# Performance work log

Hardware: AMD Instinct MI355X
Metric: run time of the kernel (lower is better)

The kernel has to match this reference:

```python
import jax, jax.numpy as jnp
import numpy as np

B, T, D = 1, 1024, 1024
H = 16; HKV = 16; HD = D // H; R = 2; K = 3; LOWR = 32
HR = HKV * R                      # heads after harmonic expansion
OUTW = HKV * HD * 2 * R           # w_proj output width
SCALE = HD ** -0.5


def setup_inputs() -> dict:
    key = jax.random.key(0)
    ks = jax.random.split(key, 10)
    def rn(k, shape, sc=1.0):
        return jax.random.normal(k, shape, dtype=jnp.float32) * sc
    return {
        'hidden_states': rn(ks[0], (B, T, D)),
        'q_w': rn(ks[1], (D, D), D ** -0.5),
        'k_w': rn(ks[2], (D, D), D ** -0.5),
        'v_w': rn(ks[3], (D, D), D ** -0.5),
        'w1': rn(ks[4], (LOWR, D), D ** -0.5),
        'w2': rn(ks[5], (OUTW, LOWR), LOWR ** -0.5),
        'conv_w': rn(ks[6], (OUTW, K), K ** -0.5),
        'bt_w': rn(ks[7], (HKV * R, D), D ** -0.5),
        'bt_b': jnp.zeros((HKV * R,), jnp.float32),
        'o_w': rn(ks[8], (D, D * R), (D * R) ** -0.5),
        'omega': 0.01 * jnp.ones((1, 1, 1, R), jnp.float32),
        'phi': jnp.zeros((1, 1, 1, R), jnp.float32),
    }


def path_attention_forward(hidden_states, q_w, k_w, v_w, w1, w2, conv_w,
                           bt_w, bt_b, o_w, omega, phi):
    b, t, _ = hidden_states.shape
    q = hidden_states @ q_w.T
    k = hidden_states @ k_w.T
    v = hidden_states @ v_w.T
    # low-rank w projection, causal depthwise short conv (kernel K), SiLU
    w_raw = (hidden_states @ w1.T) @ w2.T                    # [b,t,OUTW]
    xp = jnp.pad(w_raw, ((0, 0), (K - 1, 0), (0, 0)))
    w_raw = sum(xp[:, i:i + t, :] * conv_w[:, i] for i in range(K))
    w_raw = jax.nn.silu(w_raw)
    # rotary-like harmonic mixing of Householder directions
    w5 = w_raw.reshape(b, t, HKV, 2 * R, HD)
    Ah = w5[:, :, :, 0::2, :]                                # [b,t,HKV,R,HD]
    Bh = w5[:, :, :, 1::2, :]
    pos = jnp.arange(t, dtype=jnp.float32)[None, :, None, None]
    theta = omega * pos + phi                                # [1,t,1,R]
    c = jnp.cos(theta)[..., None]
    s = jnp.sin(theta)[..., None]
    Wdir = Ah * c + Bh * s
    Wdir = Wdir * jax.lax.rsqrt(jnp.sum(Wdir * Wdir, -1, keepdims=True) + 1e-6)
    beta = jax.nn.sigmoid(hidden_states @ bt_w.T + bt_b) * 2.0   # [b,t,HR]
    # repeat-interleave q/k/v heads across harmonics -> [b,HR,t,HD]
    to_h = lambda x: jnp.swapaxes(jnp.repeat(x.reshape(b, t, H, HD), R, axis=2), 1, 2)
    qh, kh, vh = to_h(q), to_h(k), to_h(v)
    wh = jnp.swapaxes(Wdir.reshape(b, t, HR, HD), 1, 2)      # [b,HR,t,HD]
    bh = jnp.swapaxes(beta, 1, 2)                            # [b,HR,t]
    # PaTH logits: A_ij = q_i^T (H_i ... H_{j+1}) k_j, H_t = I - beta_t w_t w_t^T.
    # WY/UT transform: with M_ts = beta_t (w_t.w_s) for s<t, the coefficients
    # B_tj (t>j) of the accumulated rank-1 corrections solve the unit-lower
    # triangular system (I + M) B = strilow(Db W K^T), and
    # A = tril(Q K^T - tril(Q W^T) B).
    idx = jnp.arange(t)
    strict = idx[:, None] > idx[None, :]
    incl = idx[:, None] >= idx[None, :]
    Mw = jnp.where(strict, jnp.einsum('bhtd,bhsd->bhts', wh, wh) * bh[..., None], 0.0)
    rhs = jnp.where(strict, jnp.einsum('bhtd,bhjd->bhtj', wh, kh) * bh[..., None], 0.0)
    Bmat = jax.scipy.linalg.solve_triangular(Mw + jnp.eye(t, dtype=Mw.dtype), rhs, lower=True)
    qk = jnp.einsum('bhid,bhjd->bhij', qh, kh)
    qw = jnp.where(incl, jnp.einsum('bhid,bhtd->bhit', qh, wh), 0.0)
    logits = (qk - jnp.einsum('bhit,bhtj->bhij', qw, Bmat)) * SCALE
    logits = jnp.where(incl, logits, -1e30)
    p = jax.nn.softmax(logits, axis=-1)
    o = jnp.einsum('bhij,bhjd->bhid', p, vh)                 # [b,HR,t,HD]
    o = jnp.swapaxes(o, 1, 2).reshape(b, t, HR * HD)         # [b,t,D*R]
    return o @ o_w.T


def reference(hidden_states, q_w, k_w, v_w, w1, w2, conv_w, bt_w, bt_b, o_w, omega, phi):
    return path_attention_forward(hidden_states, q_w, k_w, v_w, w1, w2, conv_w,
                                  bt_w, bt_b, o_w, omega, phi)
```

## Files before the change

kernel.cpp:

```cpp
#include <hip/hip_runtime.h>
#include <math.h>

#define TTD 1024
#define DDM 1024
#define HDIM 64
#define NOUTW 4096
#define PSCALE 0.125f
#define LS 72

typedef __attribute__((ext_vector_type(8))) __bf16 bf16x8;
typedef __attribute__((ext_vector_type(4))) float f32x4;
#define MFMA16(a,b,c) __builtin_amdgcn_mfma_f32_16x16x32_bf16(a,b,c,0,0,0)

__device__ __forceinline__ ushort f2b(float f) {
  unsigned u = __builtin_bit_cast(unsigned, f);
  return (ushort)((u + 0x7fffu + ((u >> 16) & 1u)) >> 16);
}
__device__ __forceinline__ float b2f(ushort u) {
  unsigned v = (unsigned)u << 16;
  return __builtin_bit_cast(float, v);
}

__device__ __forceinline__ void gload_lds16(const ushort* g, ushort* l) {
  __builtin_amdgcn_global_load_lds(
      (const __attribute__((address_space(1))) unsigned*)g,
      (__attribute__((address_space(3))) unsigned*)l, 16, 0, 0);
}

#define SWZ(row, cc) (((row) * 8 + ((cc) ^ ((row) & 7))) * 8)
#define SWZE(row, col) (SWZ(row, (col) >> 3) + ((col) & 7))

__device__ __forceinline__ void stage_tile(const ushort* gb, long gs, ushort* tile,
                                           int w, int l) {
  int sub = l >> 3, cc = (l & 7) ^ sub;
  #pragma unroll
  for (int it = 0; it < 2; ++it) {
    int q = w * 2 + it;
    gload_lds16(gb + (long)(q * 8 + sub) * gs + cc * 8, &tile[(q * 64 + l) * 8]);
  }
}

__device__ __forceinline__ bf16x8 frag(const ushort* tile, int row, int cc) {
  return *(const bf16x8*)&tile[SWZ(row, cc)];
}

#define OFF_X     0L
#define OFF_PZ    67108864L
#define OFF_HSB   67108864L
#define OFF_QWW   69206016L
#define OFF_KWW   71303168L
#define OFF_VWW   73400320L
#define OFF_W2B   75497472L
#define OFF_WLOWB 75759616L
#define OFF_TB    130023424L
#define OFF_OALL  130023424L
#define OFF_YB    134217728L
#define OFF_OWB   134217728L
#define OFF_WHB   138412032L
#define OFF_QB    142606336L
#define OFF_KB    144703488L
#define OFF_VTB   146800640L
#define OFF_BETA  148897792L
#define OFF_BW64  149159936L

__global__ __launch_bounds__(256) void cvt_kernel(const float* __restrict__ x,
                                                  ushort* __restrict__ y, long n) {
  long i = ((long)blockIdx.x * 256 + threadIdx.x) * 4;
  if (i >= n) return;
  float4 f = *(const float4*)(x + i);
  ushort4 o;
  o.x = f2b(f.x); o.y = f2b(f.y); o.z = f2b(f.z); o.w = f2b(f.w);
  *(ushort4*)(y + i) = o;
}

#define CVT_TOTAL 4358144L
struct CvtSegs {
  const float* src[6];
  ushort* dst[6];
  long cnt[6];
};
__global__ __launch_bounds__(256) void cvt_all_kernel(CvtSegs sg) {
  long e = ((long)blockIdx.x * 256 + threadIdx.x) * 4;
  #pragma unroll
  for (int s = 0; s < 6; ++s) {
    if (e < sg.cnt[s]) {
      float4 f = *(const float4*)(sg.src[s] + e);
      ushort4 o;
      o.x = f2b(f.x); o.y = f2b(f.y); o.z = f2b(f.z); o.w = f2b(f.w);
      *(ushort4*)(sg.dst[s] + e) = o;
      return;
    }
    e -= sg.cnt[s];
  }
}

__global__ __launch_bounds__(256) void qkv_sp_kernel(
    const ushort* __restrict__ hsb,
    const ushort* __restrict__ wq, const ushort* __restrict__ wk, const ushort* __restrict__ wv,
    const ushort* __restrict__ bw, const float* __restrict__ bt_b,
    ushort* __restrict__ cq, ushort* __restrict__ ck, ushort* __restrict__ cv,
    float* __restrict__ beta, ushort* __restrict__ wlowb)
{
  int z = blockIdx.z;
  if (z == 3 && blockIdx.x != 0) return;
  const ushort* B = (z == 0) ? wq : (z == 1) ? wk : (z == 2) ? wv : bw;

  __shared__ ushort Ab[2][8192];
  __shared__ ushort Bb[2][4096];

  int tid = threadIdx.x, w = tid >> 6, l = tid & 63;
  int quad = l >> 4, lane15 = l & 15;
  int rm = blockIdx.y * 128, cn = (z == 3) ? 0 : blockIdx.x * 64;
  const ushort* Ag = hsb + (long)rm * DDM;
  const ushort* Bg = B + (long)cn * DDM;

  stage_tile(Ag, DDM, &Ab[0][0], w, l);
  stage_tile(Ag + 64 * DDM, DDM, &Ab[0][4096], w, l);
  stage_tile(Bg, DDM, &Bb[0][0], w, l);
  __syncthreads();

  f32x4 acc[2][4] = {};
  int cur = 0;
  int arow0 = (w & 1) * 32 + lane15;
  int asel = (w >> 1) * 4096;
  for (int kt = 0; kt < 16; ++kt) {
    if (kt < 15) {
      stage_tile(Ag + (kt + 1) * 64, DDM, &Ab[cur ^ 1][0], w, l);
      stage_tile(Ag + 64 * DDM + (kt + 1) * 64, DDM, &Ab[cur ^ 1][4096], w, l);
      stage_tile(Bg + (kt + 1) * 64, DDM, &Bb[cur ^ 1][0], w, l);
    }
    const ushort* Atile = &Ab[cur][asel];
    #pragma unroll
    for (int s = 0; s < 2; ++s) {
      bf16x8 a0 = frag(Atile, arow0, s * 4 + quad);
      bf16x8 a1 = frag(Atile, arow0 + 16, s * 4 + quad);
      #pragma unroll
      for (int f = 0; f < 4; ++f) {
        bf16x8 bf = frag(&Bb[cur][0], f * 16 + lane15, s * 4 + quad);
        acc[0][f] = MFMA16(a0, bf, acc[0][f]);
        acc[1][f] = MFMA16(a1, bf, acc[1][f]);
      }
    }
    __syncthreads();
    cur ^= 1;
  }

  if (z < 2) {
    ushort* Cb = (z == 0) ? cq : ck;
    #pragma unroll
    for (int rr = 0; rr < 2; ++rr) {
      int orow = rm + w * 32 + rr * 16 + quad * 4;
      #pragma unroll
      for (int f = 0; f < 4; ++f)
        #pragma unroll
        for (int r = 0; r < 4; ++r)
          Cb[(long)(orow + r) * DDM + cn + f * 16 + lane15] = f2b(acc[rr][f][r]);
    }
  } else if (z == 2) {
    #pragma unroll
    for (int rr = 0; rr < 2; ++rr) {
      int orow = rm + w * 32 + rr * 16 + quad * 4;
      #pragma unroll
      for (int f = 0; f < 4; ++f) {
        ushort4 o;
        o.x = f2b(acc[rr][f][0]); o.y = f2b(acc[rr][f][1]);
        o.z = f2b(acc[rr][f][2]); o.w = f2b(acc[rr][f][3]);
        *(ushort4*)&cv[(long)(cn + f * 16 + lane15) * TTD + orow] = o;
      }
    }
  } else {
    #pragma unroll
    for (int rr = 0; rr < 2; ++rr) {
      int orow = rm + w * 32 + rr * 16 + quad * 4;
      #pragma unroll
      for (int f = 0; f < 2; ++f) {
        int hr = f * 16 + lane15;
        float bb = bt_b[hr];
        #pragma unroll
        for (int r = 0; r < 4; ++r)
          beta[(long)hr * TTD + orow + r] = 2.f / (1.f + expf(-(acc[rr][f][r] + bb)));
      }
      #pragma unroll
      for (int f = 2; f < 4; ++f)
        #pragma unroll
        for (int r = 0; r < 4; ++r)
          wlowb[(long)(orow + r) * 32 + (f - 2) * 16 + lane15] = f2b(acc[rr][f][r]);
    }
  }
}

__global__ __launch_bounds__(256) void wrawconv_kernel(
    const ushort* __restrict__ wlowb, const ushort* __restrict__ w2b,
    const float* __restrict__ conv_w, const float* __restrict__ omega,
    const float* __restrict__ phi, ushort* __restrict__ whb)
{
  int rm = blockIdx.x * 64;
  int p = blockIdx.y;
  int hkv = p >> 1, r = p & 1;
  int c0 = hkv * 256 + r * 128;

  __shared__ ushort As[64 * 32];
  __shared__ ushort Bs[128 * 32];
  __shared__ float WR[66][132];

  int tid = threadIdx.x, w = tid >> 6, l = tid & 63;
  int quad = l >> 4, lane15 = l & 15;

  {
    int row = tid >> 2, ch = (tid & 3) * 8;
    gload_lds16(wlowb + (long)(rm + row) * 32 + ch, &As[row * 32 + ch]);
    gload_lds16(w2b + (long)(c0 + row) * 32 + ch, &Bs[row * 32 + ch]);
    gload_lds16(w2b + (long)(c0 + 64 + row) * 32 + ch, &Bs[(64 + row) * 32 + ch]);
  }
  {
    int hr2 = tid >> 7, col = tid & 127;
    float acc = 0.f;
    if (rm > 0) {
      long t = rm - 2 + hr2;
      for (int k = 0; k < 32; ++k)
        acc += b2f(wlowb[t * 32 + k]) * b2f(w2b[(long)(c0 + col) * 32 + k]);
    }
    WR[hr2][col] = acc;
  }
  __syncthreads();

  #pragma unroll
  for (int g = 0; g < 2; ++g) {
    f32x4 acc[4] = {};
    bf16x8 af = *(const bf16x8*)&As[(w * 16 + lane15) * 32 + quad * 8];
    #pragma unroll
    for (int f = 0; f < 4; ++f) {
      bf16x8 bf = *(const bf16x8*)&Bs[(g * 64 + f * 16 + lane15) * 32 + quad * 8];
      acc[f] = MFMA16(af, bf, acc[f]);
    }
    #pragma unroll
    for (int f = 0; f < 4; ++f)
      #pragma unroll
      for (int rr = 0; rr < 4; ++rr)
        WR[2 + w * 16 + quad * 4 + rr][g * 64 + f * 16 + lane15] = acc[f][rr];
  }
  __syncthreads();

  float cwa[3], cwb[3];
  #pragma unroll
  for (int i = 0; i < 3; ++i) {
    cwa[i] = conv_w[(long)(c0 + l) * 3 + i];
    cwb[i] = conv_w[(long)(c0 + 64 + l) * 3 + i];
  }
  float om = omega[r], ph = phi[r];
  for (int it = 0; it < 16; ++it) {
    int tl = it * 4 + w;
    int t = rm + tl;
    float a = cwa[0] * WR[tl][l] + cwa[1] * WR[tl + 1][l] + cwa[2] * WR[tl + 2][l];
    float b = cwb[0] * WR[tl][64 + l] + cwb[1] * WR[tl + 1][64 + l] + cwb[2] * WR[tl + 2][64 + l];
    a = a / (1.f + expf(-a));
    b = b / (1.f + expf(-b));
    float th = om * (float)t + ph;
    float wd = a * cosf(th) + b * sinf(th);
    float ss = wd * wd;
    #pragma unroll
    for (int o = 32; o > 0; o >>= 1) ss += __shfl_xor(ss, o, 64);
    whb[((long)p * TTD + t) * HDIM + l] = f2b(wd * (1.f / sqrtf(ss + 1e-6f)));
  }
}

__global__ __launch_bounds__(256) void solveA_kernel(
    const ushort* __restrict__ whb, const float* __restrict__ beta,
    ushort* __restrict__ TB, ushort* __restrict__ YB)
{
  int c = blockIdx.x, h = blockIdx.y;
  const ushort* whc = whb + ((long)h * TTD + c * 64) * HDIM;
  const float* bet = beta + (long)h * TTD + c * 64;
  ushort* TBh = TB + ((long)h * 16 + c) * 4096;
  ushort* YBh = YB + ((long)h * 16 + c) * 4096;

  __shared__ float Lm[64][65];
  __shared__ float Vf[64][65];
  __shared__ ushort WT[64 * LS];
  __shared__ ushort Tb[64 * LS];

  int tid = threadIdx.x, w = tid >> 6, l = tid & 63;
  int quad = l >> 4, lane15 = l & 15;

  f32x4 g[4] = {};
  #pragma unroll
  for (int s = 0; s < 2; ++s) {
    bf16x8 af = *(const bf16x8*)&whc[(long)(w * 16 + lane15) * HDIM + s * 32 + quad * 8];
    #pragma unroll
    for (int f = 0; f < 4; ++f) {
      bf16x8 bf = *(const bf16x8*)&whc[(long)(f * 16 + lane15) * HDIM + s * 32 + quad * 8];
      g[f] = MFMA16(af, bf, g[f]);
    }
  }
  #pragma unroll
  for (int r = 0; r < 4; ++r) {
    int t = w * 16 + quad * 4 + r;
    float bv = bet[t];
    #pragma unroll
    for (int f = 0; f < 4; ++f) {
      int tp = f * 16 + lane15;
      Lm[t][tp] = (t > tp) ? bv * g[f][r] : 0.f;
    }
  }
  {
    int d0 = (tid & 7) * 8;
    #pragma unroll
    for (int it = 0; it < 2; ++it) {
      int t = it * 32 + (tid >> 3);
      uint4 pk = *(const uint4*)&whc[(long)t * HDIM + d0];
      const ushort* pu = (const ushort*)&pk;
      #pragma unroll
      for (int i = 0; i < 8; ++i) WT[(d0 + i) * LS + t] = pu[i];
    }
  }
  __syncthreads();

  {
    float cur[16];
    #pragma unroll
    for (int i = 0; i < 16; ++i) cur[i] = (w * 16 + i == l) ? bet[l] : 0.f;
    for (int sb = 0; sb < 4; ++sb) {
      if (w == sb) {
        float xloc[16];
        #pragma unroll
        for (int i = 0; i < 16; ++i) {
          float bv = cur[i];
          #pragma unroll
          for (int j2 = 0; j2 < 16; ++j2)
            if (j2 < i) bv -= Lm[sb * 16 + i][sb * 16 + j2] * xloc[j2];
          xloc[i] = bv;
          Vf[sb * 16 + i][l] = bv;
        }
      }
      __syncthreads();
      if (w > sb) {
        float xp[16];
        #pragma unroll
        for (int t = 0; t < 16; ++t) xp[t] = Vf[sb * 16 + t][l];
        #pragma unroll
        for (int i = 0; i < 16; ++i) {
          float s2 = cur[i];
          #pragma unroll
          for (int t = 0; t < 16; ++t) s2 -= Lm[w * 16 + i][sb * 16 + t] * xp[t];
          cur[i] = s2;
        }
      }
    }
  }
  {
    int t = tid >> 2, off = (tid & 3) * 16;
    ushort tmp[16];
    #pragma unroll
    for (int i = 0; i < 16; ++i) { tmp[i] = f2b(Vf[t][off + i]); Tb[t * LS + off + i] = tmp[i]; }
    *(uint4*)&TBh[t * 64 + off] = *(const uint4*)&tmp[0];
    *(uint4*)&TBh[t * 64 + off + 8] = *(const uint4*)&tmp[8];
  }
  __syncthreads();
  f32x4 y[4] = {};
  #pragma unroll
  for (int s = 0; s < 2; ++s) {
    bf16x8 af = *(const bf16x8*)&Tb[(w * 16 + lane15) * LS + s * 32 + quad * 8];
    #pragma unroll
    for (int f = 0; f < 4; ++f) {
      bf16x8 bf = *(const bf16x8*)&WT[(f * 16 + lane15) * LS + s * 32 + quad * 8];
      y[f] = MFMA16(af, bf, y[f]);
    }
  }
  #pragma unroll
  for (int f = 0; f < 4; ++f)
    #pragma unroll
    for (int r = 0; r < 4; ++r)
      YBh[(long)(w * 16 + quad * 4 + r) * 64 + f * 16 + lane15] = f2b(y[f][r]);
}

__global__ __launch_bounds__(256) void solveB_kernel(
    const ushort* __restrict__ whb, const ushort* __restrict__ kb,
    const ushort* __restrict__ TB, const ushort* __restrict__ YB,
    ushort* __restrict__ Xb, ushort* __restrict__ KZ)
{
  int h = blockIdx.x;
  int ty = blockIdx.y;
  int js = (ty < 8) ? ty : (23 - ty);
  int j0 = js * 64;
  const ushort* wh_h = whb + (long)h * TTD * HDIM;
  const ushort* k_h = kb + (long)(h >> 1) * 64;
  ushort* X_h = Xb + (long)h * TTD * TTD;
  ushort* KZ_h = KZ + (long)h * 15 * TTD * HDIM;

  __shared__ ushort KT[4096];
  __shared__ ushort WT[4096];
  __shared__ ushort XM[4096];
  __shared__ ushort nS[4096];

  int tid = threadIdx.x, w = tid >> 6, l = tid & 63;
  int quad = l >> 4, lane15 = l & 15;
  f32x4 Sacc[4] = {}, Wacc[4] = {};

  stage_tile(k_h + (long)j0 * DDM, DDM, KT, w, l);

  float kreg[4][4];
  #pragma unroll
  for (int f = 0; f < 4; ++f)
    #pragma unroll
    for (int r = 0; r < 4; ++r)
      kreg[f][r] = b2f(k_h[(long)(j0 + w * 16 + quad * 4 + r) * DDM + f * 16 + lane15]);

  for (int c = js; c < 16; ++c) {
    const ushort* whc = wh_h + (long)c * 64 * HDIM;
    __syncthreads();
    {
      int d0 = (tid & 7) * 8;
      #pragma unroll
      for (int it = 0; it < 2; ++it) {
        int t = it * 32 + (tid >> 3);
        uint4 pk = *(const uint4*)&whc[(long)t * HDIM + d0];
        const ushort* pu = (const ushort*)&pk;
        #pragma unroll
        for (int i = 0; i < 8; ++i) WT[SWZE(d0 + i, t)] = pu[i];
      }
    }
    f32x4 xacc[4] = {};
    if (c == js) {
      f32x4 m[4] = {};
      #pragma unroll
      for (int s = 0; s < 2; ++s) {
        bf16x8 af = *(const bf16x8*)&whc[(long)(w * 16 + lane15) * HDIM + s * 32 + quad * 8];
        #pragma unroll
        for (int f = 0; f < 4; ++f)
          m[f] = MFMA16(af, frag(KT, f * 16 + lane15, s * 4 + quad), m[f]);
      }
      #pragma unroll
      for (int f = 0; f < 4; ++f)
        #pragma unroll
        for (int r = 0; r < 4; ++r) {
          int t = w * 16 + quad * 4 + r, j = f * 16 + lane15;
          XM[SWZE(j, t)] = (t > j) ? f2b(m[f][r]) : (ushort)0;
        }
      __syncthreads();
      const ushort* TBh = TB + ((long)h * 16 + c) * 4096;
      #pragma unroll
      for (int s = 0; s < 2; ++s) {
        bf16x8 af = *(const bf16x8*)&TBh[(long)(w * 16 + lane15) * 64 + s * 32 + quad * 8];
        #pragma unroll
        for (int f = 0; f < 4; ++f)
          xacc[f] = MFMA16(af, frag(XM, f * 16 + lane15, s * 4 + quad), xacc[f]);
      }
      __syncthreads();
    } else {
      const ushort* YBh = YB + ((long)h * 16 + c) * 4096;
      #pragma unroll
      for (int s = 0; s < 2; ++s) {
        bf16x8 af = *(const bf16x8*)&YBh[(long)(w * 16 + lane15) * 64 + s * 32 + quad * 8];
        #pragma unroll
        for (int f = 0; f < 4; ++f) {
          xacc[f] = MFMA16(af, frag(KT, f * 16 + lane15, s * 4 + quad), xacc[f]);
          xacc[f] = MFMA16(af, frag(nS, f * 16 + lane15, s * 4 + quad), xacc[f]);
        }
      }
    }
    #pragma unroll
    for (int f = 0; f < 4; ++f)
      #pragma unroll
      for (int r = 0; r < 4; ++r)
        XM[SWZE(f * 16 + lane15, w * 16 + quad * 4 + r)] = f2b(xacc[f][r]);
    __syncthreads();
    {
      int j = tid >> 2, c2 = (tid & 3) * 2;
      bf16x8 s0 = frag(XM, j, c2);
      bf16x8 s1 = frag(XM, j, c2 + 1);
      *(bf16x8*)&X_h[(long)(j0 + j) * TTD + c * 64 + c2 * 8] = s0;
      *(bf16x8*)&X_h[(long)(j0 + j) * TTD + c * 64 + c2 * 8 + 8] = s1;
    }
    if (c < 15) {
      #pragma unroll
      for (int s = 0; s < 2; ++s) {
        bf16x8 aw = frag(WT, w * 16 + lane15, s * 4 + quad);
        bf16x8 ax = frag(XM, w * 16 + lane15, s * 4 + quad);
        #pragma unroll
        for (int f = 0; f < 4; ++f) {
          Sacc[f] = MFMA16(aw, frag(XM, f * 16 + lane15, s * 4 + quad), Sacc[f]);
          Wacc[f] = MFMA16(ax, frag(WT, f * 16 + lane15, s * 4 + quad), Wacc[f]);
        }
      }
      ushort* pz = KZ_h + (long)c * TTD * HDIM;
      #pragma unroll
      for (int f = 0; f < 4; ++f)
        #pragma unroll
        for (int r = 0; r < 4; ++r)
          pz[(long)(j0 + w * 16 + quad * 4 + r) * 64 + f * 16 + lane15] =
              f2b(kreg[f][r] - Wacc[f][r]);
      #pragma unroll
      for (int f = 0; f < 4; ++f)
        #pragma unroll
        for (int r = 0; r < 4; ++r)
          nS[SWZE(f * 16 + lane15, w * 16 + quad * 4 + r)] = f2b(-Sacc[f][r]);
    }
  }
}

__global__ __launch_bounds__(256) void flash_kernel(
    const ushort* __restrict__ qb, const ushort* __restrict__ kbuf,
    const ushort* __restrict__ whb, const ushort* __restrict__ Xb,
    const ushort* __restrict__ KZ, const ushort* __restrict__ vTb,
    ushort* __restrict__ oall)
{
  int h = blockIdx.x;
  int y = blockIdx.y;
  int ri = (y < 8) ? y : (23 - y);
  int r0 = ri * 64;
  const ushort* q_h = qb + (long)(h >> 1) * 64;
  const ushort* k_h = kbuf + (long)(h >> 1) * 64;
  const ushort* wh_h = whb + (long)h * TTD * HDIM;
  const ushort* X_h = Xb + (long)h * TTD * TTD;
  const ushort* kz = KZ + ((long)h * 15 + (ri - 1)) * TTD * HDIM;
  const ushort* v_h = vTb + (long)(h >> 1) * 64 * TTD;

  __shared__ ushort S[2][3][4096];
  __shared__ ushort KD[4096];
  __shared__ ushort QWD[4096];
  __shared__ ushort PT[4096];

  int tid = threadIdx.x, w = tid >> 6, l = tid & 63;
  int quad = l >> 4, lane15 = l & 15;

  bf16x8 aq[2];
  #pragma unroll
  for (int s = 0; s < 2; ++s)
    aq[s] = *(const bf16x8*)&q_h[(long)(r0 + w * 16 + lane15) * DDM + s * 32 + quad * 8];
  {
    f32x4 t4[4] = {};
    #pragma unroll
    for (int s = 0; s < 2; ++s)
      #pragma unroll
      for (int f = 0; f < 4; ++f) {
        bf16x8 bf = *(const bf16x8*)&wh_h[(long)(r0 + f * 16 + lane15) * HDIM + s * 32 + quad * 8];
        t4[f] = MFMA16(aq[s], bf, t4[f]);
      }
    #pragma unroll
    for (int f = 0; f < 4; ++f)
      #pragma unroll
      for (int r = 0; r < 4; ++r) {
        int i = w * 16 + quad * 4 + r, t = f * 16 + lane15;
        QWD[SWZE(i, t)] = (i >= t) ? f2b(-t4[f][r]) : (ushort)0;
      }
  }
  stage_tile(k_h + (long)r0 * DDM, DDM, KD, w, l);
  if (ri > 0) stage_tile(kz, 64, &S[0][0][0], w, l);
  stage_tile(X_h + r0, TTD, &S[0][1][0], w, l);
  stage_tile(v_h, TTD, &S[0][2][0], w, l);
  __syncthreads();

  f32x4 O[4] = {};
  float m[4], lsum[4];
  #pragma unroll
  for (int r = 0; r < 4; ++r) { m[r] = -1e30f; lsum[r] = 0.f; }

  int cur = 0;
  for (int jb = 0; jb <= ri; ++jb) {
    if (jb < ri) {
      long c0n = (long)(jb + 1) * 64;
      ushort* nb = &S[cur ^ 1][0][0];
      if (jb + 1 < ri) stage_tile(kz + c0n * 64, 64, nb, w, l);
      stage_tile(X_h + c0n * TTD + r0, TTD, nb + 4096, w, l);
      stage_tile(v_h + c0n, TTD, nb + 8192, w, l);
    }
    const ushort* Skz = &S[cur][0][0];
    const ushort* Sx  = &S[cur][1][0];
    const ushort* Sv  = &S[cur][2][0];
    f32x4 acc[4] = {};
    const ushort* Sb = (jb < ri) ? Skz : KD;
    #pragma unroll
    for (int s = 0; s < 2; ++s)
      #pragma unroll
      for (int f = 0; f < 4; ++f)
        acc[f] = MFMA16(aq[s], frag(Sb, f * 16 + lane15, s * 4 + quad), acc[f]);
    #pragma unroll
    for (int s = 0; s < 2; ++s) {
      bf16x8 aw = frag(QWD, w * 16 + lane15, s * 4 + quad);
      #pragma unroll
      for (int f = 0; f < 4; ++f)
        acc[f] = MFMA16(aw, frag(Sx, f * 16 + lane15, s * 4 + quad), acc[f]);
    }
    float rmax[4] = {-3e38f, -3e38f, -3e38f, -3e38f};
    #pragma unroll
    for (int f = 0; f < 4; ++f)
      #pragma unroll
      for (int r = 0; r < 4; ++r) {
        float lv = acc[f][r] * PSCALE;
        if (jb == ri && (f * 16 + lane15) > (w * 16 + quad * 4 + r)) lv = -3e38f;
        acc[f][r] = lv;
        rmax[r] = fmaxf(rmax[r], lv);
      }
    #pragma unroll
    for (int r = 0; r < 4; ++r) {
      rmax[r] = fmaxf(rmax[r], __shfl_xor(rmax[r], 1, 64));
      rmax[r] = fmaxf(rmax[r], __shfl_xor(rmax[r], 2, 64));
      rmax[r] = fmaxf(rmax[r], __shfl_xor(rmax[r], 4, 64));
      rmax[r] = fmaxf(rmax[r], __shfl_xor(rmax[r], 8, 64));
    }
    float alpha[4], rs[4] = {0.f, 0.f, 0.f, 0.f};
    #pragma unroll
    for (int r = 0; r < 4; ++r) {
      float nm = fmaxf(m[r], rmax[r]);
      alpha[r] = __expf(m[r] - nm);
      m[r] = nm;
    }
    #pragma unroll
    for (int f = 0; f < 4; ++f)
      #pragma unroll
      for (int r = 0; r < 4; ++r) {
        float e = __expf(acc[f][r] - m[r]);
        acc[f][r] = e;
        rs[r] += e;
      }
    #pragma unroll
    for (int r = 0; r < 4; ++r) {
      rs[r] += __shfl_xor(rs[r], 1, 64);
      rs[r] += __shfl_xor(rs[r], 2, 64);
      rs[r] += __shfl_xor(rs[r], 4, 64);
      rs[r] += __shfl_xor(rs[r], 8, 64);
      lsum[r] = lsum[r] * alpha[r] + rs[r];
    }
    #pragma unroll
    for (int f = 0; f < 4; ++f)
      #pragma unroll
      for (int r = 0; r < 4; ++r) O[f][r] *= alpha[r];
    #pragma unroll
    for (int f = 0; f < 4; ++f)
      #pragma unroll
      for (int r = 0; r < 4; ++r) {
        int i = w * 16 + quad * 4 + r;
        PT[SWZE(i, f * 16 + lane15)] = f2b(acc[f][r]);
      }
    #pragma unroll
    for (int s = 0; s < 2; ++s) {
      bf16x8 ap = frag(PT, w * 16 + lane15, s * 4 + quad);
      #pragma unroll
      for (int f = 0; f < 4; ++f)
        O[f] = MFMA16(ap, frag(Sv, f * 16 + lane15, s * 4 + quad), O[f]);
    }
    __syncthreads();
    cur ^= 1;
  }
  #pragma unroll
  for (int r = 0; r < 4; ++r) lsum[r] = 1.f / lsum[r];
  #pragma unroll
  for (int f = 0; f < 4; ++f)
    #pragma unroll
    for (int r = 0; r < 4; ++r)
      oall[(long)(r0 + w * 16 + quad * 4 + r) * 2048 + h * 64 + f * 16 + lane15] =
          f2b(O[f][r] * lsum[r]);
}

__global__ __launch_bounds__(256) void gemm_out_kernel(
    const ushort* __restrict__ A, const ushort* __restrict__ Bb, float* __restrict__ C)
{
  __shared__ ushort Ab[2][8192];
  __shared__ ushort Bt[2][8192];
  int tid = threadIdx.x, w = tid >> 6, l = tid & 63;
  int quad = l >> 4, lane15 = l & 15;
  int rm = blockIdx.y * 64, cn = blockIdx.x * 64;
  const ushort* Ag = A + (long)rm * 2048;
  const ushort* Bg = Bb + (long)cn * 2048;

  stage_tile(Ag, 2048, &Ab[0][0], w, l);
  stage_tile(Ag + 64, 2048, &Ab[0][4096], w, l);
  stage_tile(Bg, 2048, &Bt[0][0], w, l);
  stage_tile(Bg + 64, 2048, &Bt[0][4096], w, l);
  __syncthreads();

  f32x4 acc[4] = {};
  int cur = 0;
  for (int kt = 0; kt < 16; ++kt) {
    if (kt < 15) {
      long o = (long)(kt + 1) * 128;
      stage_tile(Ag + o, 2048, &Ab[cur ^ 1][0], w, l);
      stage_tile(Ag + o + 64, 2048, &Ab[cur ^ 1][4096], w, l);
      stage_tile(Bg + o, 2048, &Bt[cur ^ 1][0], w, l);
      stage_tile(Bg + o + 64, 2048, &Bt[cur ^ 1][4096], w, l);
    }
    #pragma unroll
    for (int u = 0; u < 2; ++u)
      #pragma unroll
      for (int s = 0; s < 2; ++s) {
        bf16x8 af = frag(&Ab[cur][u * 4096], w * 16 + lane15, s * 4 + quad);
        #pragma unroll
        for (int f = 0; f < 4; ++f)
          acc[f] = MFMA16(af, frag(&Bt[cur][u * 4096], f * 16 + lane15, s * 4 + quad), acc[f]);
      }
    __syncthreads();
    cur ^= 1;
  }
  int orow = rm + w * 16 + quad * 4;
  #pragma unroll
  for (int f = 0; f < 4; ++f)
    #pragma unroll
    for (int r = 0; r < 4; ++r)
      C[(long)(orow + r) * DDM + cn + f * 16 + lane15] = acc[f][r];
}

extern "C" void kernel_launch(void* const* d_in, const int* in_sizes, int n_in,
                              void* d_out, int out_size, void* d_ws, size_t ws_size,
                              hipStream_t stream) {
  const float* hs     = (const float*)d_in[0];
  const float* q_w    = (const float*)d_in[1];
  const float* k_w    = (const float*)d_in[2];
  const float* v_w    = (const float*)d_in[3];
  const float* w1     = (const float*)d_in[4];
  const float* w2     = (const float*)d_in[5];
  const float* conv_w = (const float*)d_in[6];
  const float* bt_w   = (const float*)d_in[7];
  const float* bt_b   = (const float*)d_in[8];
  const float* o_w    = (const float*)d_in[9];
  const float* omega  = (const float*)d_in[10];
  const float* phi    = (const float*)d_in[11];
  float* out = (float*)d_out;
  char* ws = (char*)d_ws;

  ushort* Xb     = (ushort*)(ws + OFF_X);
  ushort* KZb    = (ushort*)(ws + OFF_PZ);
  ushort* hs_b   = (ushort*)(ws + OFF_HSB);
  ushort* qw_wb  = (ushort*)(ws + OFF_QWW);
  ushort* kw_wb  = (ushort*)(ws + OFF_KWW);
  ushort* vw_wb  = (ushort*)(ws + OFF_VWW);
  ushort* w2_b   = (ushort*)(ws + OFF_W2B);
  ushort* wlow_b = (ushort*)(ws + OFF_WLOWB);
  ushort* TB     = (ushort*)(ws + OFF_TB);
  ushort* o_all  = (ushort*)(ws + OFF_OALL);
  ushort* YB     = (ushort*)(ws + OFF_YB);
  ushort* ow_b   = (ushort*)(ws + OFF_OWB);
  ushort* wh_b   = (ushort*)(ws + OFF_WHB);
  ushort* q_b    = (ushort*)(ws + OFF_QB);
  ushort* k_b    = (ushort*)(ws + OFF_KB);
  ushort* vT_b   = (ushort*)(ws + OFF_VTB);
  float*  beta   = (float*)(ws + OFF_BETA);
  ushort* bw_b   = (ushort*)(ws + OFF_BW64);

  CvtSegs sg;
  sg.src[0] = hs;   sg.dst[0] = hs_b;          sg.cnt[0] = 1048576;
  sg.src[1] = q_w;  sg.dst[1] = qw_wb;         sg.cnt[1] = 1048576;
  sg.src[2] = k_w;  sg.dst[2] = kw_wb;         sg.cnt[2] = 1048576;
  sg.src[3] = v_w;  sg.dst[3] = vw_wb;         sg.cnt[3] = 1048576;
  sg.src[4] = w2;   sg.dst[4] = w2_b;          sg.cnt[4] = 131072;
  sg.src[5] = bt_w; sg.dst[5] = bw_b;          sg.cnt[5] = 32768;
  cvt_all_kernel<<<dim3((CVT_TOTAL + 1023) / 1024), 256, 0, stream>>>(sg);
  cvt_kernel<<<dim3(32), 256, 0, stream>>>(w1, bw_b + 32768, 32768L);

  qkv_sp_kernel<<<dim3(16, 8, 4), 256, 0, stream>>>(
      hs_b, qw_wb, kw_wb, vw_wb, bw_b, bt_b, q_b, k_b, vT_b, beta, wlow_b);

  wrawconv_kernel<<<dim3(16, 32), 256, 0, stream>>>(
      wlow_b, w2_b, conv_w, omega, phi, wh_b);

  solveA_kernel<<<dim3(16, 32), 256, 0, stream>>>(wh_b, beta, TB, YB);
  solveB_kernel<<<dim3(32, 16), 256, 0, stream>>>(wh_b, k_b, TB, YB, Xb, KZb);

  cvt_kernel<<<dim3(2048), 256, 0, stream>>>(o_w, ow_b, 2097152L);

  flash_kernel<<<dim3(32, 16), 256, 0, stream>>>(q_b, k_b, wh_b, Xb, KZb, vT_b, o_all);

  gemm_out_kernel<<<dim3(16, 16), 256, 0, stream>>>(o_all, ow_b, out);

  (void)in_sizes; (void)n_in; (void)out_size; (void)ws_size;
}
```

Measured before the change: 237.1 us.

## Replace syncthreads with fine-grained vmcnt waits and barriers; fold w1 conversion

Result: faster. 231.6 us (-2.3%).

```diff
diff --git a/kernel.cpp b/kernel.cpp
--- a/kernel.cpp
+++ b/kernel.cpp
@@ -6,11 +6,20 @@
 #define HDIM 64
 #define NOUTW 4096
 #define PSCALE 0.125f
+#define PSC2 0.18033688011112042f
 #define LS 72
 
 typedef __attribute__((ext_vector_type(8))) __bf16 bf16x8;
 typedef __attribute__((ext_vector_type(4))) float f32x4;
 #define MFMA16(a,b,c) __builtin_amdgcn_mfma_f32_16x16x32_bf16(a,b,c,0,0,0)
+
+#define STR_(x) #x
+#define WAITVM(N) asm volatile("s_waitcnt vmcnt(" STR_(N) ")" ::: "memory")
+#define BAR() do { __builtin_amdgcn_s_barrier(); asm volatile("" ::: "memory"); } while (0)
+#define LGKBAR() do { asm volatile("s_waitcnt lgkmcnt(0)" ::: "memory"); \
+                      __builtin_amdgcn_s_barrier(); asm volatile("" ::: "memory"); } while (0)
+#define FULLBAR() do { asm volatile("s_waitcnt vmcnt(0) lgkmcnt(0)" ::: "memory"); \
+                       __builtin_amdgcn_s_barrier(); asm volatile("" ::: "memory"); } while (0)
 
 __device__ __forceinline__ ushort f2b(float f) {
   unsigned u = __builtin_bit_cast(unsigned, f);
@@ -73,16 +82,16 @@
   *(ushort4*)(y + i) = o;
 }
 
-#define CVT_TOTAL 4358144L
+#define CVT_TOTAL 4390912L
 struct CvtSegs {
-  const float* src[6];
-  ushort* dst[6];
-  long cnt[6];
+  const float* src[7];
+  ushort* dst[7];
+  long cnt[7];
 };
 __global__ __launch_bounds__(256) void cvt_all_kernel(CvtSegs sg) {
   long e = ((long)blockIdx.x * 256 + threadIdx.x) * 4;
   #pragma unroll
-  for (int s = 0; s < 6; ++s) {
+  for (int s = 0; s < 7; ++s) {
     if (e < sg.cnt[s]) {
       float4 f = *(const float4*)(sg.src[s] + e);
       ushort4 o;
@@ -117,18 +126,22 @@
   stage_tile(Ag, DDM, &Ab[0][0], w, l);
   stage_tile(Ag + 64 * DDM, DDM, &Ab[0][4096], w, l);
   stage_tile(Bg, DDM, &Bb[0][0], w, l);
-  __syncthreads();
 
   f32x4 acc[2][4] = {};
-  int cur = 0;
   int arow0 = (w & 1) * 32 + lane15;
   int asel = (w >> 1) * 4096;
   for (int kt = 0; kt < 16; ++kt) {
+    int cur = kt & 1;
     if (kt < 15) {
-      stage_tile(Ag + (kt + 1) * 64, DDM, &Ab[cur ^ 1][0], w, l);
-      stage_tile(Ag + 64 * DDM + (kt + 1) * 64, DDM, &Ab[cur ^ 1][4096], w, l);
-      stage_tile(Bg + (kt + 1) * 64, DDM, &Bb[cur ^ 1][0], w, l);
-    }
+      int nxt = cur ^ 1;
+      stage_tile(Ag + (kt + 1) * 64, DDM, &Ab[nxt][0], w, l);
+      stage_tile(Ag + 64 * DDM + (kt + 1) * 64, DDM, &Ab[nxt][4096], w, l);
+      stage_tile(Bg + (kt + 1) * 64, DDM, &Bb[nxt][0], w, l);
+      WAITVM(6);
+    } else {
+      WAITVM(0);
+    }
+    BAR();
     const ushort* Atile = &Ab[cur][asel];
     #pragma unroll
     for (int s = 0; s < 2; ++s) {
@@ -141,8 +154,7 @@
         acc[1][f] = MFMA16(a1, bf, acc[1][f]);
       }
     }
-    __syncthreads();
-    cur ^= 1;
+    BAR();
   }
 
   if (z < 2) {
@@ -222,7 +234,7 @@
     }
     WR[hr2][col] = acc;
   }
-  __syncthreads();
+  FULLBAR();
 
   #pragma unroll
   for (int g = 0; g < 2; ++g) {
@@ -239,7 +251,7 @@
       for (int rr = 0; rr < 4; ++rr)
         WR[2 + w * 16 + quad * 4 + rr][g * 64 + f * 16 + lane15] = acc[f][rr];
   }
-  __syncthreads();
+  LGKBAR();
 
   float cwa[3], cwb[3];
   #pragma unroll
@@ -313,7 +325,7 @@
       for (int i = 0; i < 8; ++i) WT[(d0 + i) * LS + t] = pu[i];
     }
   }
-  __syncthreads();
+  LGKBAR();
 
   {
     float cur[16];
@@ -332,7 +344,7 @@
           Vf[sb * 16 + i][l] = bv;
         }
       }
-      __syncthreads();
+      LGKBAR();
       if (w > sb) {
         float xp[16];
         #pragma unroll
@@ -355,7 +367,7 @@
     *(uint4*)&TBh[t * 64 + off] = *(const uint4*)&tmp[0];
     *(uint4*)&TBh[t * 64 + off + 8] = *(const uint4*)&tmp[8];
   }
-  __syncthreads();
+  LGKBAR();
   f32x4 y[4] = {};
   #pragma unroll
   for (int s = 0; s < 2; ++s) {
@@ -405,9 +417,11 @@
     for (int r = 0; r < 4; ++r)
       kreg[f][r] = b2f(k_h[(long)(j0 + w * 16 + quad * 4 + r) * DDM + f * 16 + lane15]);
 
+  WAITVM(0);
+
   for (int c = js; c < 16; ++c) {
     const ushort* whc = wh_h + (long)c * 64 * HDIM;
-    __syncthreads();
+    LGKBAR();
     {
       int d0 = (tid & 7) * 8;
       #pragma unroll
@@ -436,7 +450,7 @@
           int t = w * 16 + quad * 4 + r, j = f * 16 + lane15;
           XM[SWZE(j, t)] = (t > j) ? f2b(m[f][r]) : (ushort)0;
         }
-      __syncthreads();
+      LGKBAR();
       const ushort* TBh = TB + ((long)h * 16 + c) * 4096;
       #pragma unroll
       for (int s = 0; s < 2; ++s) {
@@ -445,7 +459,7 @@
         for (int f = 0; f < 4; ++f)
           xacc[f] = MFMA16(af, frag(XM, f * 16 + lane15, s * 4 + quad), xacc[f]);
       }
-      __syncthreads();
+      LGKBAR();
     } else {
       const ushort* YBh = YB + ((long)h * 16 + c) * 4096;
       #pragma unroll
@@ -463,7 +477,7 @@
       #pragma unroll
       for (int r = 0; r < 4; ++r)
         XM[SWZE(f * 16 + lane15, w * 16 + quad * 4 + r)] = f2b(xacc[f][r]);
-    __syncthreads();
+    LGKBAR();
     {
       int j = tid >> 2, c2 = (tid & 3) * 2;
       bf16x8 s0 = frag(XM, j, c2);
@@ -527,43 +541,52 @@
   #pragma unroll
   for (int s = 0; s < 2; ++s)
     aq[s] = *(const bf16x8*)&q_h[(long)(r0 + w * 16 + lane15) * DDM + s * 32 + quad * 8];
-  {
-    f32x4 t4[4] = {};
-    #pragma unroll
-    for (int s = 0; s < 2; ++s)
-      #pragma unroll
-      for (int f = 0; f < 4; ++f) {
-        bf16x8 bf = *(const bf16x8*)&wh_h[(long)(r0 + f * 16 + lane15) * HDIM + s * 32 + quad * 8];
-        t4[f] = MFMA16(aq[s], bf, t4[f]);
-      }
-    #pragma unroll
-    for (int f = 0; f < 4; ++f)
-      #pragma unroll
-      for (int r = 0; r < 4; ++r) {
-        int i = w * 16 + quad * 4 + r, t = f * 16 + lane15;
-        QWD[SWZE(i, t)] = (i >= t) ? f2b(-t4[f][r]) : (ushort)0;
-      }
-  }
   stage_tile(k_h + (long)r0 * DDM, DDM, KD, w, l);
   if (ri > 0) stage_tile(kz, 64, &S[0][0][0], w, l);
   stage_tile(X_h + r0, TTD, &S[0][1][0], w, l);
   stage_tile(v_h, TTD, &S[0][2][0], w, l);
-  __syncthreads();
+  {
+    f32x4 t4[4] = {};
+    #pragma unroll
+    for (int s = 0; s < 2; ++s)
+      #pragma unroll
+      for (int f = 0; f < 4; ++f) {
+        bf16x8 bf = *(const bf16x8*)&wh_h[(long)(r0 + f * 16 + lane15) * HDIM + s * 32 + quad * 8];
+        t4[f] = MFMA16(aq[s], bf, t4[f]);
+      }
+    #pragma unroll
+    for (int f = 0; f < 4; ++f)
+      #pragma unroll
+      for (int r = 0; r < 4; ++r) {
+        int i = w * 16 + quad * 4 + r, t = f * 16 + lane15;
+        QWD[SWZE(i, t)] = (i >= t) ? f2b(-t4[f][r]) : (ushort)0;
+      }
+  }
 
   f32x4 O[4] = {};
   float m[4], lsum[4];
   #pragma unroll
   for (int r = 0; r < 4; ++r) { m[r] = -1e30f; lsum[r] = 0.f; }
 
-  int cur = 0;
   for (int jb = 0; jb <= ri; ++jb) {
+    int cur = jb & 1;
     if (jb < ri) {
       long c0n = (long)(jb + 1) * 64;
       ushort* nb = &S[cur ^ 1][0][0];
-      if (jb + 1 < ri) stage_tile(kz + c0n * 64, 64, nb, w, l);
-      stage_tile(X_h + c0n * TTD + r0, TTD, nb + 4096, w, l);
-      stage_tile(v_h + c0n, TTD, nb + 8192, w, l);
-    }
+      if (jb + 1 < ri) {
+        stage_tile(kz + c0n * 64, 64, nb, w, l);
+        stage_tile(X_h + c0n * TTD + r0, TTD, nb + 4096, w, l);
+        stage_tile(v_h + c0n, TTD, nb + 8192, w, l);
+        WAITVM(6);
+      } else {
+        stage_tile(X_h + c0n * TTD + r0, TTD, nb + 4096, w, l);
+        stage_tile(v_h + c0n, TTD, nb + 8192, w, l);
+        WAITVM(4);
+      }
+    } else {
+      WAITVM(0);
+    }
+    BAR();
     const ushort* Skz = &S[cur][0][0];
     const ushort* Sx  = &S[cur][1][0];
     const ushort* Sv  = &S[cur][2][0];
@@ -586,7 +609,7 @@
     for (int f = 0; f < 4; ++f)
       #pragma unroll
       for (int r = 0; r < 4; ++r) {
-        float lv = acc[f][r] * PSCALE;
+        float lv = acc[f][r] * PSC2;
         if (jb == ri && (f * 16 + lane15) > (w * 16 + quad * 4 + r)) lv = -3e38f;
         acc[f][r] = lv;
         rmax[r] = fmaxf(rmax[r], lv);
@@ -602,14 +625,14 @@
     #pragma unroll
     for (int r = 0; r < 4; ++r) {
       float nm = fmaxf(m[r], rmax[r]);
-      alpha[r] = __expf(m[r] - nm);
+      alpha[r] = exp2f(m[r] - nm);
       m[r] = nm;
     }
     #pragma unroll
     for (int f = 0; f < 4; ++f)
       #pragma unroll
       for (int r = 0; r < 4; ++r) {
-        float e = __expf(acc[f][r] - m[r]);
+        float e = exp2f(acc[f][r] - m[r]);
         acc[f][r] = e;
         rs[r] += e;
       }
@@ -639,8 +662,7 @@
       for (int f = 0; f < 4; ++f)
         O[f] = MFMA16(ap, frag(Sv, f * 16 + lane15, s * 4 + quad), O[f]);
     }
-    __syncthreads();
-    cur ^= 1;
+    BAR();
   }
   #pragma unroll
   for (int r = 0; r < 4; ++r) lsum[r] = 1.f / lsum[r];
@@ -667,18 +689,22 @@
   stage_tile(Ag + 64, 2048, &Ab[0][4096], w, l);
   stage_tile(Bg, 2048, &Bt[0][0], w, l);
   stage_tile(Bg + 64, 2048, &Bt[0][4096], w, l);
-  __syncthreads();
 
   f32x4 acc[4] = {};
-  int cur = 0;
   for (int kt = 0; kt < 16; ++kt) {
+    int cur = kt & 1;
     if (kt < 15) {
+      int nxt = cur ^ 1;
       long o = (long)(kt + 1) * 128;
-      stage_tile(Ag + o, 2048, &Ab[cur ^ 1][0], w, l);
-      stage_tile(Ag + o + 64, 2048, &Ab[cur ^ 1][4096], w, l);
-      stage_tile(Bg + o, 2048, &Bt[cur ^ 1][0], w, l);
-      stage_tile(Bg + o + 64, 2048, &Bt[cur ^ 1][4096], w, l);
-    }
+      stage_tile(Ag + o, 2048, &Ab[nxt][0], w, l);
+      stage_tile(Ag + o + 64, 2048, &Ab[nxt][4096], w, l);
+      stage_tile(Bg + o, 2048, &Bt[nxt][0], w, l);
+      stage_tile(Bg + o + 64, 2048, &Bt[nxt][4096], w, l);
+      WAITVM(8);
+    } else {
+      WAITVM(0);
+    }
+    BAR();
     #pragma unroll
     for (int u = 0; u < 2; ++u)
       #pragma unroll
@@ -688,8 +714,7 @@
         for (int f = 0; f < 4; ++f)
           acc[f] = MFMA16(af, frag(&Bt[cur][u * 4096], f * 16 + lane15, s * 4 + quad), acc[f]);
       }
-    __syncthreads();
-    cur ^= 1;
+    BAR();
   }
   int orow = rm + w * 16 + quad * 4;
   #pragma unroll
@@ -743,8 +768,8 @@
   sg.src[3] = v_w;  sg.dst[3] = vw_wb;         sg.cnt[3] = 1048576;
   sg.src[4] = w2;   sg.dst[4] = w2_b;          sg.cnt[4] = 131072;
   sg.src[5] = bt_w; sg.dst[5] = bw_b;          sg.cnt[5] = 32768;
+  sg.src[6] = w1;   sg.dst[6] = bw_b + 32768;  sg.cnt[6] = 32768;
   cvt_all_kernel<<<dim3((CVT_TOTAL + 1023) / 1024), 256, 0, stream>>>(sg);
-  cvt_kernel<<<dim3(32), 256, 0, stream>>>(w1, bw_b + 32768, 32768L);
 
   qkv_sp_kernel<<<dim3(16, 8, 4), 256, 0, stream>>>(
       hs_b, qw_wb, kw_wb, vw_wb, bw_b, bt_b, q_b, k_b, vT_b, beta, wlow_b);
```
